# Kernel tuning notes

Hardware: AMD Instinct MI355X
Metric: run time of the kernel (lower is better)

The kernel has to match this reference:

```python
import jax, jax.numpy as jnp
from jax import lax
import numpy as np

MAX_ITER = 50
BAND_WIDTH = 3.0
MIN_BAND_VOXELS = 32
EPS = 1e-06


def _chamfer(mask_f):
    # mask_f: [N, H, W] float in {0,1}. Iterative 3x3 max-pool dilation; a pixel
    # newly reached at iteration i gets distance i (matches torch max_pool2d loop).
    # Running the full MAX_ITER iterations is equivalent to the early break:
    # once no new pixels appear, dist is never updated again.
    def body(i, carry):
        dist, cur = carry
        dil = lax.reduce_window(cur, -jnp.inf, lax.max, (1, 3, 3), (1, 1, 1), 'SAME')
        new = (dil > 0) & (cur == 0)
        dist = jnp.where(new, i.astype(dist.dtype), dist)
        return (dist, dil)

    dist0 = jnp.zeros_like(mask_f)
    dist, _ = lax.fori_loop(1, MAX_ITER + 1, body, (dist0, mask_f))
    return dist


def _signed_distance(m):
    # m: [N, H, W] float binary masks. Positive outside, negative inside.
    H, W = m.shape[-2], m.shape[-1]
    sdm = _chamfer(m) - _chamfer(1.0 - m)
    msum = m.sum((-2, -1))
    trivial = (msum == 0) | (msum == H * W)  # all-empty or all-full -> zeros
    return jnp.where(trivial[:, None, None], 0.0, sdm)


def setup_inputs() -> dict:
    key = jax.random.key(0)
    k1, k2 = jax.random.split(key)
    B, C, H, W = 8, 4, 512, 512
    probs = jax.random.uniform(k1, (B, C, H, W), dtype=jnp.float32)
    target = jax.random.randint(k2, (B, H, W), 0, C, dtype=jnp.int64)
    return {"probs": probs, "target": target}


def reference(probs, target):
    B, C, H, W = probs.shape
    probs = probs.astype(jnp.float32)
    # one-hot [B, C, H, W] bool; default include_background=False -> classes 1..C-1
    one_hot = target[:, None, :, :] == jnp.arange(C, dtype=target.dtype)[None, :, None, None]
    m = one_hot[:, 1:].astype(jnp.float32).reshape(B * (C - 1), H, W)
    p = probs[:, 1:].reshape(B * (C - 1), H, W)

    d = jnp.abs(_signed_distance(m))          # [N, H, W]
    band = (d <= BAND_WIDTH).astype(jnp.float32)
    denom = band.sum((-2, -1))                 # [N]

    err = jnp.abs(p - m)                       # L1 (error_power=1.0)
    loss_bc = (err * d * band).sum((-2, -1)) / (denom + EPS)

    include = (denom >= MIN_BAND_VOXELS).astype(jnp.float32)
    count = include.sum()
    return (loss_bc * include).sum() / (count + EPS)
```

## Files before the change

### kernel.cpp

```cpp
#include <hip/hip_runtime.h>


#define HH 512
#define WW 512
#define BB 8
#define STRIP 8
#define SROWS (STRIP + 6)
#define NBLK 512


__global__ __launch_bounds__(256) void gsl_stage1(
    const float* __restrict__ probs,
    const int*   __restrict__ target,
    float* __restrict__ ws)
{
    __shared__ uint4 hrow[SROWS * 64];
    __shared__ float redf[4][3];
    __shared__ int   redi[4][3];

    const int tid   = threadIdx.x;
    const int lane  = tid & 63;
    const int wave  = tid >> 6;
    const int strip = blockIdx.x;
    const int b     = blockIdx.y;
    const int y0    = strip * STRIP;
    const int* __restrict__ tgt_b = target + b * (HH * WW);

    #pragma unroll
    for (int i = 0; i < 4; ++i) {
        const int ri = wave + 4 * i;
        if (ri < SROWS) {
            const int gy = y0 - 3 + ri;
            uint32_t wv = 0u, h1 = 0u, h2 = 0u, h3 = 0u;
            if ((unsigned)gy < (unsigned)HH) {
                const int4* trow = (const int4*)(tgt_b + gy * WW);
                const int4 t0 = trow[lane * 2];
                const int4 t1 = trow[lane * 2 + 1];
                wv = (1u << t0.x)        | (1u << (t0.y + 4))
                   | (1u << (t0.z + 8))  | (1u << (t0.w + 12))
                   | (1u << (t1.x + 16)) | (1u << (t1.y + 20))
                   | (1u << (t1.z + 24)) | (1u << (t1.w + 28));
                uint32_t wl = __shfl_up(wv, 1, 64);   if (lane == 0)  wl = 0u;
                uint32_t wr = __shfl_down(wv, 1, 64); if (lane == 63) wr = 0u;
                h1 = wv | ((wv << 4)  | (wl >> 28)) | ((wv >> 4)  | (wr << 28));
                h2 = h1 | ((wv << 8)  | (wl >> 24)) | ((wv >> 8)  | (wr << 24));
                h3 = h2 | ((wv << 12) | (wl >> 20)) | ((wv >> 12) | (wr << 20));
            }
            hrow[ri * 64 + lane] = make_uint4(h1, h2, h3, wv);
        }
    }
    __syncthreads();

    float num[3] = {0.f, 0.f, 0.f};
    int   den[3] = {0, 0, 0};
    int   mc [3] = {0, 0, 0};

    #pragma unroll
    for (int t = 0; t < 2; ++t) {
        const int yo = wave * 2 + t;
        const int gy = y0 + yo;
        const int lr = yo + 3;

        const float4* pr1 = (const float4*)(probs + (size_t)(((b * 4) + 1) * HH + gy) * WW);
        const float4* pr2 = (const float4*)(probs + (size_t)(((b * 4) + 2) * HH + gy) * WW);
        const float4* pr3 = (const float4*)(probs + (size_t)(((b * 4) + 3) * HH + gy) * WW);
        const float4 f1a = pr1[lane * 2], f1b = pr1[lane * 2 + 1];
        const float4 f2a = pr2[lane * 2], f2b = pr2[lane * 2 + 1];
        const float4 f3a = pr3[lane * 2], f3b = pr3[lane * 2 + 1];

        const uint4 r0 = hrow[(lr - 3) * 64 + lane];
        const uint4 r1 = hrow[(lr - 2) * 64 + lane];
        const uint4 r2 = hrow[(lr - 1) * 64 + lane];
        const uint4 r3 = hrow[(lr    ) * 64 + lane];
        const uint4 r4 = hrow[(lr + 1) * 64 + lane];
        const uint4 r5 = hrow[(lr + 2) * 64 + lane];
        const uint4 r6 = hrow[(lr + 3) * 64 + lane];
        const uint32_t p1 = r2.x | r3.x | r4.x;
        const uint32_t p2 = r1.y | r2.y | r3.y | r4.y | r5.y;
        const uint32_t p3 = r0.z | r1.z | r2.z | r3.z | r4.z | r5.z | r6.z;
        const uint32_t cw = r3.w;

        const float pv[3][8] = {
            {f1a.x, f1a.y, f1a.z, f1a.w, f1b.x, f1b.y, f1b.z, f1b.w},
            {f2a.x, f2a.y, f2a.z, f2a.w, f2b.x, f2b.y, f2b.z, f2b.w},
            {f3a.x, f3a.y, f3a.z, f3a.w, f3b.x, f3b.y, f3b.z, f3b.w}};

        #pragma unroll
        for (int j = 0; j < 8; ++j) {
            const uint32_t q1 = (p1 >> (4 * j)) & 15u;
            const uint32_t q2 = (p2 >> (4 * j)) & 15u;
            const uint32_t q3 = (p3 >> (4 * j)) & 15u;
            const uint32_t cb = (cw >> (4 * j)) & 15u;
            #pragma unroll
            for (int k = 0; k < 3; ++k) {
                const uint32_t cm = 2u << k;
                const bool v = (cb & cm) != 0u;
                const uint32_t sel = v ? (15u & ~cm) : cm;
                const uint32_t a1 = q1 & sel;
                const uint32_t a2 = q2 & sel;
                const uint32_t a3 = q3 & sel;
                const float df  = a1 ? 1.f : (a2 ? 2.f : 3.f);
                const float err = fabsf(pv[k][j] - (v ? 1.f : 0.f));
                num[k] += a3 ? err * df : 0.f;
                den[k] += a3 ? 1 : 0;
                mc [k] += v  ? 1 : 0;
            }
        }
    }

    int pk0 = den[0] | (den[1] << 16);
    int pk1 = den[2] | (mc[0] << 16);
    int pk2 = mc[1]  | (mc[2] << 16);
    #pragma unroll
    for (int off = 32; off; off >>= 1) {
        num[0] += __shfl_down(num[0], off, 64);
        num[1] += __shfl_down(num[1], off, 64);
        num[2] += __shfl_down(num[2], off, 64);
        pk0    += __shfl_down(pk0,    off, 64);
        pk1    += __shfl_down(pk1,    off, 64);
        pk2    += __shfl_down(pk2,    off, 64);
    }
    if (lane == 0) {
        redf[wave][0] = num[0]; redf[wave][1] = num[1]; redf[wave][2] = num[2];
        redi[wave][0] = pk0;    redi[wave][1] = pk1;    redi[wave][2] = pk2;
    }
    __syncthreads();
    if (tid == 0) {
        const int blockFlat = b * 64 + strip;
        float n0 = 0.f, n1 = 0.f, n2 = 0.f;
        int s0 = 0, s1 = 0, s2 = 0;
        #pragma unroll
        for (int w = 0; w < 4; ++w) {
            n0 += redf[w][0]; n1 += redf[w][1]; n2 += redf[w][2];
            s0 += redi[w][0]; s1 += redi[w][1]; s2 += redi[w][2];
        }
        ws[(0 * 3 + 0) * NBLK + blockFlat] = n0;
        ws[(0 * 3 + 1) * NBLK + blockFlat] = n1;
        ws[(0 * 3 + 2) * NBLK + blockFlat] = n2;
        ws[(1 * 3 + 0) * NBLK + blockFlat] = (float)(s0 & 0xFFFF);
        ws[(1 * 3 + 1) * NBLK + blockFlat] = (float)(s0 >> 16);
        ws[(1 * 3 + 2) * NBLK + blockFlat] = (float)(s1 & 0xFFFF);
        ws[(2 * 3 + 0) * NBLK + blockFlat] = (float)(s1 >> 16);
        ws[(2 * 3 + 1) * NBLK + blockFlat] = (float)(s2 & 0xFFFF);
        ws[(2 * 3 + 2) * NBLK + blockFlat] = (float)(s2 >> 16);
    }
}

__global__ __launch_bounds__(1024) void gsl_finish(
    const float* __restrict__ ws, float* __restrict__ out)
{
    __shared__ float ws2[72];
    const int tid = threadIdx.x, lane = tid & 63, wave = tid >> 6;

    for (int g = wave; g < 72; g += 16) {
        const int grp = g / 24, rem = g - grp * 24;
        const int bb = rem / 3, cc = rem - bb * 3;
        float s = ws[(grp * 3 + cc) * NBLK + bb * 64 + lane];
        #pragma unroll
        for (int off = 32; off; off >>= 1) s += __shfl_down(s, off, 64);
        if (lane == 0) ws2[g] = s;
    }
    __syncthreads();

    if (wave == 0) {
        float loss = 0.f, incl = 0.f;
        if (lane < 24) {
            const float num = ws2[lane];
            const float den = ws2[24 + lane];
            const float mcv = ws2[48 + lane];
            const bool trivial = (mcv == 0.f) || (mcv == (float)(HH * WW));
            if (trivial) {
                incl = 1.f; loss = 0.f;
            } else if (den >= 32.f) {
                incl = 1.f;
                loss = num / (den + 1e-6f);
            }
        }
        #pragma unroll
        for (int off = 32; off; off >>= 1) {
            loss += __shfl_down(loss, off, 64);
            incl += __shfl_down(incl, off, 64);
        }
        if (lane == 0) out[0] = loss / (incl + 1e-6f);
    }
}

extern "C" void kernel_launch(void* const* d_in, const int* in_sizes, int n_in,
                              void* d_out, int out_size, void* d_ws, size_t ws_size,
                              hipStream_t stream)
{
    const float* probs  = (const float*)d_in[0];
    const int*   target = (const int*)d_in[1];
    float* out = (float*)d_out;
    float* ws  = (float*)d_ws;

    dim3 grid1(64, BB);
    gsl_stage1<<<grid1, 256, 0, stream>>>(probs, target, ws);
    gsl_finish<<<1, 1024, 0, stream>>>(ws, out);
}
```

Before: 84.81 us.

## Use one wave per output row and prefetch probs before target staging

```diff
diff --git a/kernel.cpp b/kernel.cpp
--- a/kernel.cpp
+++ b/kernel.cpp
@@ -9,14 +9,14 @@
 #define NBLK 512
 
 
-__global__ __launch_bounds__(256) void gsl_stage1(
+__global__ __launch_bounds__(512) void gsl_stage1(
     const float* __restrict__ probs,
     const int*   __restrict__ target,
     float* __restrict__ ws)
 {
     __shared__ uint4 hrow[SROWS * 64];
-    __shared__ float redf[4][3];
-    __shared__ int   redi[4][3];
+    __shared__ float redf[8][3];
+    __shared__ int   redi[8][3];
 
     const int tid   = threadIdx.x;
     const int lane  = tid & 63;
@@ -24,16 +24,24 @@
     const int strip = blockIdx.x;
     const int b     = blockIdx.y;
     const int y0    = strip * STRIP;
+    const int gy    = y0 + wave;
     const int* __restrict__ tgt_b = target + b * (HH * WW);
 
-    #pragma unroll
-    for (int i = 0; i < 4; ++i) {
-        const int ri = wave + 4 * i;
+    const float4* pr1 = (const float4*)(probs + (size_t)(((b * 4) + 1) * HH + gy) * WW);
+    const float4* pr2 = (const float4*)(probs + (size_t)(((b * 4) + 2) * HH + gy) * WW);
+    const float4* pr3 = (const float4*)(probs + (size_t)(((b * 4) + 3) * HH + gy) * WW);
+    const float4 f1a = pr1[lane * 2], f1b = pr1[lane * 2 + 1];
+    const float4 f2a = pr2[lane * 2], f2b = pr2[lane * 2 + 1];
+    const float4 f3a = pr3[lane * 2], f3b = pr3[lane * 2 + 1];
+
+    #pragma unroll
+    for (int i = 0; i < 2; ++i) {
+        const int ri = wave + 8 * i;
         if (ri < SROWS) {
-            const int gy = y0 - 3 + ri;
+            const int gyt = y0 - 3 + ri;
             uint32_t wv = 0u, h1 = 0u, h2 = 0u, h3 = 0u;
-            if ((unsigned)gy < (unsigned)HH) {
-                const int4* trow = (const int4*)(tgt_b + gy * WW);
+            if ((unsigned)gyt < (unsigned)HH) {
+                const int4* trow = (const int4*)(tgt_b + gyt * WW);
                 const int4 t0 = trow[lane * 2];
                 const int4 t1 = trow[lane * 2 + 1];
                 wv = (1u << t0.x)        | (1u << (t0.y + 4))
@@ -51,60 +59,47 @@
     }
     __syncthreads();
 
+    const int lr = wave + 3;
+    const uint4 r0 = hrow[(lr - 3) * 64 + lane];
+    const uint4 r1 = hrow[(lr - 2) * 64 + lane];
+    const uint4 r2 = hrow[(lr - 1) * 64 + lane];
+    const uint4 r3 = hrow[(lr    ) * 64 + lane];
+    const uint4 r4 = hrow[(lr + 1) * 64 + lane];
+    const uint4 r5 = hrow[(lr + 2) * 64 + lane];
+    const uint4 r6 = hrow[(lr + 3) * 64 + lane];
+    const uint32_t p1 = r2.x | r3.x | r4.x;
+    const uint32_t p2 = r1.y | r2.y | r3.y | r4.y | r5.y;
+    const uint32_t p3 = r0.z | r1.z | r2.z | r3.z | r4.z | r5.z | r6.z;
+    const uint32_t cw = r3.w;
+
+    const float pv[3][8] = {
+        {f1a.x, f1a.y, f1a.z, f1a.w, f1b.x, f1b.y, f1b.z, f1b.w},
+        {f2a.x, f2a.y, f2a.z, f2a.w, f2b.x, f2b.y, f2b.z, f2b.w},
+        {f3a.x, f3a.y, f3a.z, f3a.w, f3b.x, f3b.y, f3b.z, f3b.w}};
+
     float num[3] = {0.f, 0.f, 0.f};
     int   den[3] = {0, 0, 0};
     int   mc [3] = {0, 0, 0};
 
     #pragma unroll
-    for (int t = 0; t < 2; ++t) {
-        const int yo = wave * 2 + t;
-        const int gy = y0 + yo;
-        const int lr = yo + 3;
-
-        const float4* pr1 = (const float4*)(probs + (size_t)(((b * 4) + 1) * HH + gy) * WW);
-        const float4* pr2 = (const float4*)(probs + (size_t)(((b * 4) + 2) * HH + gy) * WW);
-        const float4* pr3 = (const float4*)(probs + (size_t)(((b * 4) + 3) * HH + gy) * WW);
-        const float4 f1a = pr1[lane * 2], f1b = pr1[lane * 2 + 1];
-        const float4 f2a = pr2[lane * 2], f2b = pr2[lane * 2 + 1];
-        const float4 f3a = pr3[lane * 2], f3b = pr3[lane * 2 + 1];
-
-        const uint4 r0 = hrow[(lr - 3) * 64 + lane];
-        const uint4 r1 = hrow[(lr - 2) * 64 + lane];
-        const uint4 r2 = hrow[(lr - 1) * 64 + lane];
-        const uint4 r3 = hrow[(lr    ) * 64 + lane];
-        const uint4 r4 = hrow[(lr + 1) * 64 + lane];
-        const uint4 r5 = hrow[(lr + 2) * 64 + lane];
-        const uint4 r6 = hrow[(lr + 3) * 64 + lane];
-        const uint32_t p1 = r2.x | r3.x | r4.x;
-        const uint32_t p2 = r1.y | r2.y | r3.y | r4.y | r5.y;
-        const uint32_t p3 = r0.z | r1.z | r2.z | r3.z | r4.z | r5.z | r6.z;
-        const uint32_t cw = r3.w;
-
-        const float pv[3][8] = {
-            {f1a.x, f1a.y, f1a.z, f1a.w, f1b.x, f1b.y, f1b.z, f1b.w},
-            {f2a.x, f2a.y, f2a.z, f2a.w, f2b.x, f2b.y, f2b.z, f2b.w},
-            {f3a.x, f3a.y, f3a.z, f3a.w, f3b.x, f3b.y, f3b.z, f3b.w}};
-
-        #pragma unroll
-        for (int j = 0; j < 8; ++j) {
-            const uint32_t q1 = (p1 >> (4 * j)) & 15u;
-            const uint32_t q2 = (p2 >> (4 * j)) & 15u;
-            const uint32_t q3 = (p3 >> (4 * j)) & 15u;
-            const uint32_t cb = (cw >> (4 * j)) & 15u;
-            #pragma unroll
-            for (int k = 0; k < 3; ++k) {
-                const uint32_t cm = 2u << k;
-                const bool v = (cb & cm) != 0u;
-                const uint32_t sel = v ? (15u & ~cm) : cm;
-                const uint32_t a1 = q1 & sel;
-                const uint32_t a2 = q2 & sel;
-                const uint32_t a3 = q3 & sel;
-                const float df  = a1 ? 1.f : (a2 ? 2.f : 3.f);
-                const float err = fabsf(pv[k][j] - (v ? 1.f : 0.f));
-                num[k] += a3 ? err * df : 0.f;
-                den[k] += a3 ? 1 : 0;
-                mc [k] += v  ? 1 : 0;
-            }
+    for (int j = 0; j < 8; ++j) {
+        const uint32_t q1 = (p1 >> (4 * j)) & 15u;
+        const uint32_t q2 = (p2 >> (4 * j)) & 15u;
+        const uint32_t q3 = (p3 >> (4 * j)) & 15u;
+        const uint32_t cb = (cw >> (4 * j)) & 15u;
+        #pragma unroll
+        for (int k = 0; k < 3; ++k) {
+            const uint32_t cm = 2u << k;
+            const bool v = (cb & cm) != 0u;
+            const uint32_t sel = v ? (15u & ~cm) : cm;
+            const uint32_t a1 = q1 & sel;
+            const uint32_t a2 = q2 & sel;
+            const uint32_t a3 = q3 & sel;
+            const float df  = a1 ? 1.f : (a2 ? 2.f : 3.f);
+            const float err = fabsf(pv[k][j] - (v ? 1.f : 0.f));
+            num[k] += a3 ? err * df : 0.f;
+            den[k] += a3 ? 1 : 0;
+            mc [k] += v  ? 1 : 0;
         }
     }
 
@@ -130,7 +125,7 @@
         float n0 = 0.f, n1 = 0.f, n2 = 0.f;
         int s0 = 0, s1 = 0, s2 = 0;
         #pragma unroll
-        for (int w = 0; w < 4; ++w) {
+        for (int w = 0; w < 8; ++w) {
             n0 += redf[w][0]; n1 += redf[w][1]; n2 += redf[w][2];
             s0 += redi[w][0]; s1 += redi[w][1]; s2 += redi[w][2];
         }
@@ -152,13 +147,27 @@
     __shared__ float ws2[72];
     const int tid = threadIdx.x, lane = tid & 63, wave = tid >> 6;
 
-    for (int g = wave; g < 72; g += 16) {
-        const int grp = g / 24, rem = g - grp * 24;
-        const int bb = rem / 3, cc = rem - bb * 3;
-        float s = ws[(grp * 3 + cc) * NBLK + bb * 64 + lane];
-        #pragma unroll
-        for (int off = 32; off; off >>= 1) s += __shfl_down(s, off, 64);
-        if (lane == 0) ws2[g] = s;
+    float s[5];
+    #pragma unroll
+    for (int i = 0; i < 5; ++i) {
+        const int g = wave * 5 + i;
+        if (g < 72) {
+            const int grp = g / 24, rem = g - grp * 24;
+            const int bb = rem / 3, cc = rem - bb * 3;
+            s[i] = ws[(grp * 3 + cc) * NBLK + bb * 64 + lane];
+        } else s[i] = 0.f;
+    }
+    #pragma unroll
+    for (int i = 0; i < 5; ++i) {
+        #pragma unroll
+        for (int off = 32; off; off >>= 1) s[i] += __shfl_down(s[i], off, 64);
+    }
+    if (lane == 0) {
+        #pragma unroll
+        for (int i = 0; i < 5; ++i) {
+            const int g = wave * 5 + i;
+            if (g < 72) ws2[g] = s[i];
+        }
     }
     __syncthreads();
 
@@ -195,6 +204,6 @@
     float* ws  = (float*)d_ws;
 
     dim3 grid1(64, BB);
-    gsl_stage1<<<grid1, 256, 0, stream>>>(probs, target, ws);
+    gsl_stage1<<<grid1, 512, 0, stream>>>(probs, target, ws);
     gsl_finish<<<1, 1024, 0, stream>>>(ws, out);
 }
```

Result: no change. 85.62 us (+1.0%).
